# Performance work log

Hardware: AMD Instinct MI355X
Metric: run time of the kernel (lower is better)

The kernel has to match this reference:

```python
import jax, jax.numpy as jnp
import numpy as np

EPS_DIR = 1e-15
EPS_W = 1e-5
NEAR_MIN = 0.05


def setup_inputs() -> dict:
    key = jax.random.key(0)
    k1, k2, k3 = jax.random.split(key, 3)
    B, N, T = 1, 262144, 128
    rays_o = jax.random.normal(k1, (B, N, 3), dtype=jnp.float32)
    rays_d = jax.random.normal(k2, (B, N, 3), dtype=jnp.float32)
    weights = jax.random.uniform(k3, (B * N, T - 1), dtype=jnp.float32)
    return {"rays_o": rays_o, "rays_d": rays_d, "weights": weights,
            "bound": 1, "n_samples": 128}


def _near_far_cube(ro, rd, bound):
    # ro, rd: [R, 3]
    tmin = (-bound - ro) / (rd + EPS_DIR)
    tmax = (bound - ro) / (rd + EPS_DIR)
    near = jnp.max(jnp.minimum(tmin, tmax), axis=-1, keepdims=True)  # [R,1]
    far = jnp.min(jnp.maximum(tmin, tmax), axis=-1, keepdims=True)   # [R,1]
    near = jnp.maximum(near, NEAR_MIN)
    return near, far


def _sample_pdf(bins, weights, n_samples):
    # bins: [R, T], weights: [R, T-1]; deterministic (det=True) inverse-CDF sampling
    w = weights + EPS_W
    pdf = w / jnp.sum(w, axis=-1, keepdims=True)
    cdf = jnp.cumsum(pdf, axis=-1)
    cdf = jnp.concatenate([jnp.zeros_like(cdf[..., :1]), cdf], axis=-1)  # [R, T]
    n = n_samples
    u = jnp.linspace(0.5 / n, 1.0 - 0.5 / n, n, dtype=cdf.dtype)
    u = jnp.broadcast_to(u, cdf.shape[:-1] + (n,))                        # [R, n]
    inds = jax.vmap(lambda c, uu: jnp.searchsorted(c, uu, side='right'))(cdf, u)
    T = cdf.shape[-1]
    below = jnp.maximum(inds - 1, 0)
    above = jnp.minimum(inds, T - 1)
    cdf_lo = jnp.take_along_axis(cdf, below, axis=-1)
    cdf_hi = jnp.take_along_axis(cdf, above, axis=-1)
    bin_lo = jnp.take_along_axis(bins, below, axis=-1)
    bin_hi = jnp.take_along_axis(bins, above, axis=-1)
    denom = cdf_hi - cdf_lo
    denom = jnp.where(denom < EPS_W, jnp.ones_like(denom), denom)
    t = (u - cdf_lo) / denom
    return bin_lo + t * (bin_hi - bin_lo)  # [R, n]


def reference(rays_o, rays_d, weights, bound, n_samples):
    ro = rays_o.reshape(-1, 3)
    rd = rays_d.reshape(-1, 3)
    near, far = _near_far_cube(ro, rd, float(bound))          # [R,1]
    T = weights.shape[-1] + 1
    z = jnp.linspace(0.0, 1.0, T, dtype=ro.dtype)[None, :]    # [1,T]
    z_vals = near + (far - near) * z                          # [R,T] coarse bins
    new_z_vals = _sample_pdf(z_vals, weights, n_samples)      # [R,n_samples]
    return new_z_vals
```

## Files before the change

kernel.cpp:

```cpp
#include <hip/hip_runtime.h>

#define EPS_DIR 1e-15f
#define EPS_W   1e-5f
#define NEAR_MIN 0.05f

__global__ __launch_bounds__(256) void nerf_sample_pdf_127_128(
    const float* __restrict__ rays_o,
    const float* __restrict__ rays_d,
    const float* __restrict__ weights,
    const int*   __restrict__ bound_p,
    float*       __restrict__ out,
    int R)
{
    const int t    = threadIdx.x;
    const int g    = t & 7;
    const int rloc = t >> 3;
    int ray = blockIdx.x * 32 + rloc;
    const bool valid = (ray < R);
    if (!valid) ray = R - 1;

    __shared__ float cdf_s[32 * 132];
    float* __restrict__ cdf = cdf_s + rloc * 132;

    const float* __restrict__ wrow = weights + (size_t)ray * 127;
    const int i0 = g << 4;
    float w[16];
#pragma unroll
    for (int k = 0; k < 16; ++k) {
        const int i = i0 + k;
        w[k] = (i < 127) ? (wrow[i] + EPS_W) : 0.0f;
    }

    float local = w[0];
#pragma unroll
    for (int k = 1; k < 16; ++k) local += w[k];

    float prefix = 0.0f, val = local;
#pragma unroll
    for (int k = 1; k < 8; k <<= 1) {
        const float y = __shfl_xor(val, k, 8);
        if (g & k) prefix += y;
        val += y;
    }
    const float rtot = __builtin_amdgcn_rcpf(val);

    if (g == 0) cdf[0] = 0.0f;
    float run = prefix;
#pragma unroll
    for (int k = 0; k < 16; ++k) {
        run += w[k];
        cdf[i0 + k + 1] = run * rtot;
    }

    const float b = (float)bound_p[0];
    float nearv = -3.4e38f, farv = 3.4e38f;
#pragma unroll
    for (int k = 0; k < 3; ++k) {
        const float o = rays_o[(size_t)ray * 3 + k];
        const float d = rays_d[(size_t)ray * 3 + k] + EPS_DIR;
        const float r = __builtin_amdgcn_rcpf(d);
        const float t0 = (-b - o) * r;
        const float t1 = ( b - o) * r;
        nearv = fmaxf(nearv, fminf(t0, t1));
        farv  = fminf(farv,  fmaxf(t0, t1));
    }
    nearv = fmaxf(nearv, NEAR_MIN);
    const float scale = (farv - nearv) * (1.0f / 127.0f);

    float* __restrict__ orow = out + (size_t)ray * 128;
    const float inv_n = 1.0f / 128.0f;

#pragma unroll
    for (int q = 0; q < 4; ++q) {
        float z0, z1, z2, z3;
#pragma unroll
        for (int s = 0; s < 4; ++s) {
            const int j = i0 + 4 * q + s;
            const float u = ((float)j + 0.5f) * inv_n;
            int p = 0; float v = 0.0f;
#pragma unroll
            for (int step = 64; step >= 1; step >>= 1) {
                const float c = cdf[p + step];
                if (c <= u) { p += step; v = c; }
            }
            const float h   = cdf[p + 1];
            const float dnm = h - v;
            const float rd  = (dnm < EPS_W) ? 1.0f : __builtin_amdgcn_rcpf(dnm);
            const float tt  = (u - v) * rd;
            const float z   = fmaf((float)p + tt, scale, nearv);
            if      (s == 0) z0 = z;
            else if (s == 1) z1 = z;
            else if (s == 2) z2 = z;
            else             z3 = z;
        }
        if (valid) {
            *reinterpret_cast<float4*>(orow + i0 + 4 * q) =
                make_float4(z0, z1, z2, z3);
        }
    }
}

__global__ __launch_bounds__(256) void nerf_sample_pdf_generic(
    const float* __restrict__ rays_o,
    const float* __restrict__ rays_d,
    const float* __restrict__ weights,
    const int*   __restrict__ bound_p,
    float*       __restrict__ out,
    int R, int Tm1, int n)
{
    const int lane = threadIdx.x & 63;
    const int wid  = threadIdx.x >> 6;
    int ray = blockIdx.x * 4 + wid;
    const bool valid = (ray < R);
    if (!valid) ray = R - 1;

    __shared__ float cdf_s[4][132];
    float* __restrict__ cdf = cdf_s[wid];

    const float* __restrict__ wrow = weights + (size_t)ray * Tm1;
    const int i0 = 2 * lane, i1 = 2 * lane + 1;
    float w0 = (i0 < Tm1) ? (wrow[i0] + EPS_W) : 0.0f;
    float w1 = (i1 < Tm1) ? (wrow[i1] + EPS_W) : 0.0f;

    float S = w0 + w1;
#pragma unroll
    for (int off = 1; off < 64; off <<= 1) {
        float y = __shfl_up(S, off, 64);
        if (lane >= off) S += y;
    }
    const float total = __shfl(S, 63, 64);
    const float rinv  = __builtin_amdgcn_rcpf(total);
    float prevS = __shfl_up(S, 1, 64);
    if (lane == 0) prevS = 0.0f;

    cdf[i0] = prevS * rinv;
    cdf[i1] = (prevS + w0) * rinv;
    __syncthreads();

    const float b = (float)bound_p[0];
    float nearv = -3.4e38f, farv = 3.4e38f;
#pragma unroll
    for (int k = 0; k < 3; ++k) {
        float o = rays_o[(size_t)ray * 3 + k];
        float d = rays_d[(size_t)ray * 3 + k] + EPS_DIR;
        float r = __builtin_amdgcn_rcpf(d);
        float t0 = (-b - o) * r;
        float t1 = ( b - o) * r;
        nearv = fmaxf(nearv, fminf(t0, t1));
        farv  = fminf(farv,  fmaxf(t0, t1));
    }
    nearv = fmaxf(nearv, NEAR_MIN);
    const float scale = (farv - nearv) * __builtin_amdgcn_rcpf((float)Tm1);
    const float inv_n = 1.0f / (float)n;

    float* __restrict__ orow = out + (size_t)ray * n;

    for (int base = 0; base < n; base += 128) {
        const int j = base + 2 * lane;
        if (j >= n) break;
        const float u0 = ((float)j + 0.5f) * inv_n;
        const float u1 = u0 + inv_n;

        int   p0 = 0,   p1 = 0;
        float v0 = 0.f, v1 = 0.f;
#pragma unroll
        for (int step = 64; step >= 1; step >>= 1) {
            if (p0 + step <= Tm1) {
                const float c0 = cdf[p0 + step];
                if (c0 <= u0) { p0 += step; v0 = c0; }
            }
            if (p1 + step <= Tm1) {
                const float c1 = cdf[p1 + step];
                if (c1 <= u1) { p1 += step; v1 = c1; }
            }
        }
        const int a0 = (p0 < Tm1) ? p0 + 1 : Tm1;
        const int a1 = (p1 < Tm1) ? p1 + 1 : Tm1;
        const float h0 = cdf[a0];
        const float h1 = cdf[a1];
        const float d0 = h0 - v0;
        const float d1 = h1 - v1;
        const float t0 = (u0 - v0) * ((d0 < EPS_W) ? 1.0f : __builtin_amdgcn_rcpf(d0));
        const float t1 = (u1 - v1) * ((d1 < EPS_W) ? 1.0f : __builtin_amdgcn_rcpf(d1));
        const float z0 = fmaf(t0, (float)(a0 - p0) * scale, fmaf((float)p0, scale, nearv));
        const float z1 = fmaf(t1, (float)(a1 - p1) * scale, fmaf((float)p1, scale, nearv));

        if (valid) {
            if (j + 1 < n) {
                *reinterpret_cast<float2*>(orow + j) = make_float2(z0, z1);
            } else {
                orow[j] = z0;
            }
        }
    }
}

extern "C" void kernel_launch(void* const* d_in, const int* in_sizes, int n_in,
                              void* d_out, int out_size, void* d_ws, size_t ws_size,
                              hipStream_t stream) {
    const float* rays_o  = (const float*)d_in[0];
    const float* rays_d  = (const float*)d_in[1];
    const float* weights = (const float*)d_in[2];
    const int*   bound_p = (const int*)d_in[3];
    float*       out     = (float*)d_out;

    const int R   = in_sizes[0] / 3;
    const int Tm1 = in_sizes[2] / R;
    const int n   = out_size / R;

    if (Tm1 == 127 && n == 128) {
        dim3 grid((R + 31) / 32), block(256);
        nerf_sample_pdf_127_128<<<grid, block, 0, stream>>>(
            rays_o, rays_d, weights, bound_p, out, R);
    } else {
        dim3 grid((R + 3) / 4), block(256);
        nerf_sample_pdf_generic<<<grid, block, 0, stream>>>(
            rays_o, rays_d, weights, bound_p, out, R, Tm1, n);
    }
}
```

Baseline: 258.1 us.

## Replace per-sample binary search with per-thread merge over owned CDF segment

Each of the 8 threads per ray now keeps its 16 CDF values in registers and computes which output samples fall into its CDF range. It then emits those samples with a linear merge walk instead of a shared-memory binary search for each output. This removes the LDS traffic and the 7-step search per sample. In exchange, threads do different amounts of work, their loops diverge, the output stores become scalar and uncoalesced instead of float4, and results may differ slightly at bin boundaries because of how the float index is computed with ceil.

```diff
diff --git a/kernel.cpp b/kernel.cpp
--- a/kernel.cpp
+++ b/kernel.cpp
@@ -19,9 +19,6 @@
     const bool valid = (ray < R);
     if (!valid) ray = R - 1;
 
-    __shared__ float cdf_s[32 * 132];
-    float* __restrict__ cdf = cdf_s + rloc * 132;
-
     const float* __restrict__ wrow = weights + (size_t)ray * 127;
     const int i0 = g << 4;
     float w[16];
@@ -42,15 +39,16 @@
         if (g & k) prefix += y;
         val += y;
     }
-    const float rtot = __builtin_amdgcn_rcpf(val);
-
-    if (g == 0) cdf[0] = 0.0f;
-    float run = prefix;
-#pragma unroll
-    for (int k = 0; k < 16; ++k) {
-        run += w[k];
-        cdf[i0 + k + 1] = run * rtot;
-    }
+    const float rtot  = __builtin_amdgcn_rcpf(val);
+    const float pnext = __shfl_down(prefix, 1, 8);
+
+    float ch[16];
+    {
+        float run = prefix;
+#pragma unroll
+        for (int k = 0; k < 16; ++k) { run += w[k]; ch[k] = run * rtot; }
+    }
+    const float c_lo0 = prefix * rtot;
 
     const float b = (float)bound_p[0];
     float nearv = -3.4e38f, farv = 3.4e38f;
@@ -67,36 +65,41 @@
     nearv = fmaxf(nearv, NEAR_MIN);
     const float scale = (farv - nearv) * (1.0f / 127.0f);
 
+    int j0 = (int)ceilf(fmaf(128.0f, c_lo0, -0.5f));
+    if (j0 < 0) j0 = 0;
+    int jend;
+    if (g == 7) {
+        jend = 128;
+    } else {
+        jend = (int)ceilf(fmaf(128.0f, pnext * rtot, -0.5f));
+        if (jend > 128) jend = 128;
+    }
+    if (!valid) { j0 = 0; jend = 0; }
+
     float* __restrict__ orow = out + (size_t)ray * 128;
     const float inv_n = 1.0f / 128.0f;
 
-#pragma unroll
-    for (int q = 0; q < 4; ++q) {
-        float z0, z1, z2, z3;
-#pragma unroll
-        for (int s = 0; s < 4; ++s) {
-            const int j = i0 + 4 * q + s;
-            const float u = ((float)j + 0.5f) * inv_n;
-            int p = 0; float v = 0.0f;
-#pragma unroll
-            for (int step = 64; step >= 1; step >>= 1) {
-                const float c = cdf[p + step];
-                if (c <= u) { p += step; v = c; }
-            }
-            const float h   = cdf[p + 1];
-            const float dnm = h - v;
-            const float rd  = (dnm < EPS_W) ? 1.0f : __builtin_amdgcn_rcpf(dnm);
-            const float tt  = (u - v) * rd;
-            const float z   = fmaf((float)p + tt, scale, nearv);
-            if      (s == 0) z0 = z;
-            else if (s == 1) z1 = z;
-            else if (s == 2) z2 = z;
-            else             z3 = z;
+    int   j    = j0;
+    float u    = fmaf((float)j, inv_n, 0.5f * inv_n);
+    float c_lo = c_lo0;
+#pragma unroll
+    for (int k = 0; k < 16; ++k) {
+        const float c_hi = ch[k];
+        const float dnm  = c_hi - c_lo;
+        const float rd   = (dnm < EPS_W) ? 1.0f : __builtin_amdgcn_rcpf(dnm);
+        const float zb   = fmaf((float)(i0 + k), scale, nearv);
+        if (k < 15) {
+            while (j < jend && u < c_hi) {
+                orow[j] = fmaf((u - c_lo) * rd, scale, zb);
+                ++j; u += inv_n;
+            }
+        } else {
+            while (j < jend) {
+                orow[j] = fmaf((u - c_lo) * rd, scale, zb);
+                ++j; u += inv_n;
+            }
         }
-        if (valid) {
-            *reinterpret_cast<float4*>(orow + i0 + 4 * q) =
-                make_float4(z0, z1, z2, z3);
-        }
+        c_lo = c_hi;
     }
 }
 
```

Measured after the change: 351.7 us. +36.2%, slower.

## Stage weights through LDS with coalesced loads and reuse binary search across samples

Applied to the files above, without the earlier changes.

Each wavefront now loads its 8 rays' weights with a contiguous, coalesced loop into a shared buffer. Before, each thread read 16 scattered floats from global memory. The same buffer is then reused in place for the CDF after a barrier. The sample loop does one binary search per group of 4 consecutive samples and walks forward linearly for the rest, which cuts LDS search traffic. Output writes are interleaved across threads for better coalescing. The cost is an added __syncthreads and data-dependent while loops that can cause divergence.

```diff
diff --git a/kernel.cpp b/kernel.cpp
--- a/kernel.cpp
+++ b/kernel.cpp
@@ -13,22 +13,38 @@
     int R)
 {
     const int t    = threadIdx.x;
+    const int lane = t & 63;
+    const int wv   = t >> 6;
     const int g    = t & 7;
+    const int rw   = lane >> 3;
     const int rloc = t >> 3;
-    int ray = blockIdx.x * 32 + rloc;
+    const int ray  = blockIdx.x * 32 + rloc;
     const bool valid = (ray < R);
-    if (!valid) ray = R - 1;
-
-    __shared__ float cdf_s[32 * 132];
-    float* __restrict__ cdf = cdf_s + rloc * 132;
-
-    const float* __restrict__ wrow = weights + (size_t)ray * 127;
+    const int rayc = valid ? ray : (R - 1);
+
+    __shared__ float buf_s[4][1072];
+    float* __restrict__ wbuf = buf_s[wv];
+
+    {
+        const int ray0 = blockIdx.x * 32 + wv * 8;
+        const size_t gbase = (size_t)ray0 * 127;
+        const size_t total = (size_t)R * 127;
+#pragma unroll
+        for (int k = 0; k < 16; ++k) {
+            const int idx = 64 * k + lane;
+            if (idx < 1016) {
+                const size_t gi = gbase + (size_t)idx;
+                wbuf[idx] = (gi < total) ? weights[gi] : 0.0f;
+            }
+        }
+    }
+
     const int i0 = g << 4;
     float w[16];
 #pragma unroll
     for (int k = 0; k < 16; ++k) {
-        const int i = i0 + k;
-        w[k] = (i < 127) ? (wrow[i] + EPS_W) : 0.0f;
+        const float rv = wbuf[127 * rw + i0 + k];
+        w[k] = (i0 + k < 127) ? rv + EPS_W : 0.0f;
     }
 
     float local = w[0];
@@ -44,20 +60,25 @@
     }
     const float rtot = __builtin_amdgcn_rcpf(val);
 
+    __syncthreads();
+
+    float* __restrict__ cdf = wbuf + 133 * rw;
     if (g == 0) cdf[0] = 0.0f;
-    float run = prefix;
-#pragma unroll
-    for (int k = 0; k < 16; ++k) {
-        run += w[k];
-        cdf[i0 + k + 1] = run * rtot;
+    {
+        float run = prefix;
+#pragma unroll
+        for (int k = 0; k < 16; ++k) {
+            run += w[k];
+            cdf[i0 + k + 1] = run * rtot;
+        }
     }
 
     const float b = (float)bound_p[0];
     float nearv = -3.4e38f, farv = 3.4e38f;
 #pragma unroll
     for (int k = 0; k < 3; ++k) {
-        const float o = rays_o[(size_t)ray * 3 + k];
-        const float d = rays_d[(size_t)ray * 3 + k] + EPS_DIR;
+        const float o = rays_o[(size_t)rayc * 3 + k];
+        const float d = rays_d[(size_t)rayc * 3 + k] + EPS_DIR;
         const float r = __builtin_amdgcn_rcpf(d);
         const float t0 = (-b - o) * r;
         const float t1 = ( b - o) * r;
@@ -71,31 +92,32 @@
     const float inv_n = 1.0f / 128.0f;
 
 #pragma unroll
-    for (int q = 0; q < 4; ++q) {
+    for (int i = 0; i < 4; ++i) {
+        const int jb = 32 * i + 4 * g;
+        float u = ((float)jb + 0.5f) * inv_n;
+        int   p = 0;
+        float v = 0.0f;
+#pragma unroll
+        for (int step = 64; step >= 1; step >>= 1) {
+            const float c = cdf[p + step];
+            if (c <= u) { p += step; v = c; }
+        }
+        float h = cdf[p + 1];
         float z0, z1, z2, z3;
 #pragma unroll
         for (int s = 0; s < 4; ++s) {
-            const int j = i0 + 4 * q + s;
-            const float u = ((float)j + 0.5f) * inv_n;
-            int p = 0; float v = 0.0f;
-#pragma unroll
-            for (int step = 64; step >= 1; step >>= 1) {
-                const float c = cdf[p + step];
-                if (c <= u) { p += step; v = c; }
-            }
-            const float h   = cdf[p + 1];
+            while (h <= u && p < 127) { ++p; v = h; h = cdf[p + 1]; }
             const float dnm = h - v;
             const float rd  = (dnm < EPS_W) ? 1.0f : __builtin_amdgcn_rcpf(dnm);
-            const float tt  = (u - v) * rd;
-            const float z   = fmaf((float)p + tt, scale, nearv);
+            const float z   = fmaf((float)p + (u - v) * rd, scale, nearv);
             if      (s == 0) z0 = z;
             else if (s == 1) z1 = z;
             else if (s == 2) z2 = z;
             else             z3 = z;
+            u += inv_n;
         }
         if (valid) {
-            *reinterpret_cast<float4*>(orow + i0 + 4 * q) =
-                make_float4(z0, z1, z2, z3);
+            *reinterpret_cast<float4*>(orow + jb) = make_float4(z0, z1, z2, z3);
         }
     }
 }
```

Result: slower. 276.9 us (+7.3%).
